# Optimization experiments

Measured on AMD Instinct MI355X. Metric: run time of the kernel, lower is better.

Reference implementation:

```python
import jax, jax.numpy as jnp
import numpy as np

BS, TS, NE, ED = 32, 64, 64, 96
E = 256        # attn_embed_dim
H = 4          # attn_n_heads
HD = E // H    # head dim
RNN_H = 256
N_ACT = 32
NA = 16        # n_agents


def setup_inputs():
    key = jax.random.key(0)
    ks = jax.random.split(key, 40)
    entities = jax.random.normal(ks[0], (BS, TS, NE, ED), jnp.float32)
    obs_mask = jax.random.randint(ks[1], (BS, TS, NE, NE), 0, 2).astype(jnp.float32)  # 1 = masked
    entity_mask = (jax.random.uniform(ks[2], (BS, TS, NE)) < 0.1).astype(jnp.float32)  # 1 = inactive
    hidden_state = jnp.zeros((BS * NA, RNN_H), jnp.float32)
    it = iter(range(3, 40))
    def lin(fi, fo):
        return jax.random.normal(ks[next(it)], (fi, fo), jnp.float32) / np.sqrt(fi).astype(np.float32)
    p = dict(
        fc1_w=lin(ED, E), fc1_b=jnp.zeros((E,), jnp.float32),
        attn_in_w=lin(E, 3 * E), attn_out_w=lin(E, E), attn_out_b=jnp.zeros((E,), jnp.float32),
        fc2_w=lin(2 * E, RNN_H), fc2_b=jnp.zeros((RNN_H,), jnp.float32),
        gru_w_ih=lin(RNN_H, 3 * RNN_H), gru_w_hh=lin(RNN_H, 3 * RNN_H),
        gru_b_ih=jnp.zeros((3 * RNN_H,), jnp.float32), gru_b_hh=jnp.zeros((3 * RNN_H,), jnp.float32),
        fc3_w=lin(RNN_H, N_ACT), fc3_b=jnp.zeros((N_ACT,), jnp.float32),
        fcmsg1_w=lin(ED, E), fcmsg1_b=jnp.zeros((E,), jnp.float32),
        lmsg_in_w=lin(E, 3 * E), lmsg_out_w=lin(E, E), lmsg_out_b=jnp.zeros((E,), jnp.float32),
        gmsg_in_w=lin(E, 3 * E), gmsg_out_w=lin(E, E), gmsg_out_b=jnp.zeros((E,), jnp.float32),
        gate_in_w=lin(E, 3 * E), gate_out_w=lin(E, E), gate_out_b=jnp.zeros((E,), jnp.float32),
        gatefc1_w=lin(ED, E), gatefc1_b=jnp.zeros((E,), jnp.float32),
        gatefc2_w=lin(E, 2), gatefc2_b=jnp.zeros((2,), jnp.float32),
    )
    return dict(entities=entities, obs_mask=obs_mask, entity_mask=entity_mask,
                hidden_state=hidden_state, **p)


def _attn(x, in_w, out_w, out_b, pre_mask, post_mask):
    """REFIL EntityAttentionLayer: n_queries = NA agent rows, masks use 1 = masked."""
    B, ne, e = x.shape
    q, k, v = jnp.split(x @ in_w, 3, axis=-1)                       # each [B, ne, E]
    q = q[:, :NA].reshape(B, NA, H, HD).transpose(0, 2, 1, 3)        # [B, H, NA, HD]
    k = k.reshape(B, ne, H, HD).transpose(0, 2, 1, 3)                # [B, H, ne, HD]
    v = v.reshape(B, ne, H, HD).transpose(0, 2, 1, 3)
    logits = jnp.einsum('bhqd,bhkd->bhqk', q, k) / jnp.asarray(np.sqrt(HD), x.dtype)
    m = pre_mask[:, None, :NA, :]                                    # [B, 1, NA, ne]
    logits = jnp.where(m > 0, jnp.asarray(-1e9, x.dtype), logits)
    # softmax; zeroing masked cols also reproduces torch's NaN->0 for fully-masked rows
    w = jax.nn.softmax(logits, axis=-1) * (1.0 - m)
    out = jnp.einsum('bhqk,bhkd->bhqd', w, v).transpose(0, 2, 1, 3).reshape(B, NA, e)
    out = out @ out_w + out_b
    return out * (1.0 - post_mask[..., None])                        # masked_fill(post_mask, 0)


def _forward(entities, obs_mask, entity_mask, hidden_state,
             fc1_w, fc1_b, attn_in_w, attn_out_w, attn_out_b, fc2_w, fc2_b,
             gru_w_ih, gru_w_hh, gru_b_ih, gru_b_hh, fc3_w, fc3_b,
             fcmsg1_w, fcmsg1_b, lmsg_in_w, lmsg_out_w, lmsg_out_b,
             gmsg_in_w, gmsg_out_w, gmsg_out_b, gate_in_w, gate_out_w, gate_out_b,
             gatefc1_w, gatefc1_b, gatefc2_w, gatefc2_b):
    bs, ts, ne, ed = entities.shape
    B = bs * ts
    ent = entities.reshape(B, ne, ed)
    om = obs_mask.reshape(B, ne, ne)
    em = entity_mask.reshape(B, ne)
    agent_mask = em[:, :NA]                                          # [B, NA]
    full_obs_mask = 1.0 - (1.0 - agent_mask[:, None, :]) * (1.0 - agent_mask[:, :, None])

    x1 = jax.nn.relu(ent @ fc1_w + fc1_b)
    x2 = _attn(x1, attn_in_w, attn_out_w, attn_out_b, om, agent_mask)          # [B, NA, E]

    x1_msg = jax.nn.relu(ent @ fcmsg1_w + fcmsg1_b)
    x1_gate = jax.nn.relu(ent @ gatefc1_w + gatefc1_b)
    x2_msg = _attn(x1_msg, lmsg_in_w, lmsg_out_w, lmsg_out_b, om, agent_mask)  # [B, NA, E]
    x2_gate = _attn(x1_gate, gate_in_w, gate_out_w, gate_out_b, om, agent_mask)
    x2_gate = x2_gate @ gatefc2_w + gatefc2_b                                   # [B, NA, 2]

    # argmax of softmax == argmax of logits; gate in {0,1}, non-differentiable
    gate = jnp.argmax(x2_gate, axis=-1).astype(entities.dtype)
    gated_msg = x2_msg * gate[..., None]
    global_msg = _attn(gated_msg, gmsg_in_w, gmsg_out_w, gmsg_out_b,
                       full_obs_mask, agent_mask)                               # [B, NA, E]

    x3 = jax.nn.relu(jnp.concatenate([x2, global_msg], axis=-1) @ fc2_w + fc2_b)
    x3 = x3.reshape(bs, ts, NA, RNN_H)

    # GRU recurrence over ts via scan; hidden flattened to [bs*NA, RNN_H]
    h0 = hidden_state.reshape(-1, RNN_H)
    xs = x3.transpose(1, 0, 2, 3).reshape(ts, bs * NA, RNN_H)

    def step(h, x):
        gi = x @ gru_w_ih + gru_b_ih
        gh = h @ gru_w_hh + gru_b_hh
        ir, iz, inn = jnp.split(gi, 3, axis=-1)
        hr, hz, hn = jnp.split(gh, 3, axis=-1)
        r = jax.nn.sigmoid(ir + hr)
        z = jax.nn.sigmoid(iz + hz)
        n = jnp.tanh(inn + r * hn)
        h_new = (1.0 - z) * n + z * h
        return h_new, h_new

    _, hs = jax.lax.scan(step, h0, xs)                               # [ts, bs*NA, RNN_H]
    hs = hs.reshape(ts, bs, NA, RNN_H).transpose(1, 0, 2, 3)         # [bs, ts, NA, RNN_H]

    q = hs @ fc3_w + fc3_b                                           # [bs, ts, NA, N_ACT]
    am = agent_mask.reshape(bs, ts, NA, 1)
    q = q * (1.0 - am)                                               # masked_fill(agent_mask, 0)
    return q, hs, x2_gate


def reference(entities, obs_mask, entity_mask, hidden_state,
              fc1_w, fc1_b, attn_in_w, attn_out_w, attn_out_b, fc2_w, fc2_b,
              gru_w_ih, gru_w_hh, gru_b_ih, gru_b_hh, fc3_w, fc3_b,
              fcmsg1_w, fcmsg1_b, lmsg_in_w, lmsg_out_w, lmsg_out_b,
              gmsg_in_w, gmsg_out_w, gmsg_out_b, gate_in_w, gate_out_w, gate_out_b,
              gatefc1_w, gatefc1_b, gatefc2_w, gatefc2_b):
    return _forward(entities, obs_mask, entity_mask, hidden_state,
                    fc1_w, fc1_b, attn_in_w, attn_out_w, attn_out_b, fc2_w, fc2_b,
                    gru_w_ih, gru_w_hh, gru_b_ih, gru_b_hh, fc3_w, fc3_b,
                    fcmsg1_w, fcmsg1_b, lmsg_in_w, lmsg_out_w, lmsg_out_b,
                    gmsg_in_w, gmsg_out_w, gmsg_out_b, gate_in_w, gate_out_w, gate_out_b,
                    gatefc1_w, gatefc1_b, gatefc2_w, gatefc2_b)
```

## Files before the change

kernel.cpp:

```cpp
#include <hip/hip_runtime.h>


#define DEV __device__ __forceinline__

typedef _Float16 f16x8 __attribute__((ext_vector_type(8)));
typedef _Float16 f16x4 __attribute__((ext_vector_type(4)));
typedef float    f32x4 __attribute__((ext_vector_type(4)));
typedef float    f32x16 __attribute__((ext_vector_type(16)));

DEV f32x4 mfma16(f16x8 a, f16x8 b, f32x4 c){
  return __builtin_amdgcn_mfma_f32_16x16x32_f16(a, b, c, 0, 0, 0);
}
DEV f32x16 mfma32(f16x8 a, f16x8 b, f32x16 c){
  return __builtin_amdgcn_mfma_f32_32x32x16_f16(a, b, c, 0, 0, 0);
}

template<int MODE> struct AB {
  f16x8 hi, lo;
  DEV void mf(const AB& b, f32x4& c) const {
    if constexpr (MODE){
      c = mfma16(lo, b.hi, c);
      c = mfma16(hi, b.lo, c);
    }
    c = mfma16(hi, b.hi, c);
  }
};

template<int MODE> DEV AB<MODE> ldW(const _Float16* p, int losz){
  AB<MODE> r; r.hi = *(const f16x8*)p;
  if constexpr (MODE) r.lo = *(const f16x8*)(p + losz);
  return r;
}
template<int MODE> DEV AB<MODE> ldL(const _Float16* ph, const _Float16* pl){
  AB<MODE> r; r.hi = *(const f16x8*)ph;
  if constexpr (MODE) r.lo = *(const f16x8*)pl;
  return r;
}
template<int MODE> DEV AB<MODE> ldF(const float* p){
  AB<MODE> r;
  f32x4 v0 = *(const f32x4*)p, v1 = *(const f32x4*)(p + 4);
#pragma unroll
  for (int i = 0; i < 4; ++i){
    float a = v0[i], b = v1[i];
    _Float16 ah = (_Float16)a, bh = (_Float16)b;
    r.hi[i] = ah; r.hi[i+4] = bh;
    if constexpr (MODE){
      r.lo[i]   = (_Float16)(a - (float)ah);
      r.lo[i+4] = (_Float16)(b - (float)bh);
    }
  }
  return r;
}
template<int MODE> DEV void stL(_Float16* ph, _Float16* pl, int idx, float v){
  _Float16 h = (_Float16)v;
  ph[idx] = h;
  if constexpr (MODE) pl[idx] = (_Float16)(v - (float)h);
}

struct WJobs {
  const float* src[15];
  unsigned off[15];
  int K[15], N[15], mode[15];
};

__global__ __launch_bounds__(256) void k0_conv(WJobs jb, char* ws){
  const int job = blockIdx.y;
  const int K = jb.K[job], N = jb.N[job];
  const int total = K * N;
  _Float16* dh = (_Float16*)(ws + jb.off[job]);
  const float* src = jb.src[job];
  const int m = jb.mode[job];
  for (int idx = blockIdx.x*256 + threadIdx.x; idx < total; idx += gridDim.x*256){
    int n = idx / K, k = idx - n*K;
    float v = src[(size_t)k*N + n];
    _Float16 h = (_Float16)v;
    dh[idx] = h;
    if (m) dh[total + idx] = (_Float16)(v - (float)h);
  }
}

__global__ __launch_bounds__(256) void k0w_gate(
    const float* __restrict__ Wout, const float* __restrict__ Wg2,
    const float* __restrict__ bo,   const float* __restrict__ Win,
    _Float16* __restrict__ wveff, float* __restrict__ beff)
{
  __shared__ float weff_s[256*2];
  const int tid = threadIdx.x;
  {
    float a0 = 0.f, a1 = 0.f;
    const float* wr = Wout + (size_t)tid*256;
    for (int f = 0; f < 256; ++f){ float x = wr[f]; a0 += x*Wg2[2*f]; a1 += x*Wg2[2*f+1]; }
    weff_s[tid*2] = a0; weff_s[tid*2+1] = a1;
  }
  if (tid < 2){
    float s = 0.f;
    for (int f = 0; f < 256; ++f) s += bo[f]*Wg2[2*f + tid];
    beff[tid] = s;
  }
  __syncthreads();
  {
    const int j = tid;
    for (int n = 0; n < 16; ++n){
      float v = 0.f;
      if (n < 8){
        int h = n >> 1, c = n & 1;
        const float* wr = Win + (size_t)j*768 + 512 + h*64;
        const float* we = weff_s + (h*64)*2 + c;
        for (int d = 0; d < 64; ++d) v += wr[d]*we[2*d];
      }
      _Float16 hi = (_Float16)v;
      wveff[n*256 + j] = hi;
      wveff[16*256 + n*256 + j] = (_Float16)(v - (float)hi);
    }
  }
}

__global__ __launch_bounds__(512) void k1_all(
    const float* __restrict__ ent, const float* __restrict__ om, const float* __restrict__ em,
    const _Float16* __restrict__ W1a, const float* __restrict__ b1a,
    const _Float16* __restrict__ WINa,
    const _Float16* __restrict__ WOUTa, const float* __restrict__ boa,
    float* __restrict__ x2outa,
    const _Float16* __restrict__ W1b, const float* __restrict__ b1b,
    const _Float16* __restrict__ WINb,
    const _Float16* __restrict__ WOUTb, const float* __restrict__ bob,
    float* __restrict__ x2outb,
    const _Float16* __restrict__ W1g, const float* __restrict__ b1g,
    const _Float16* __restrict__ WINg,
    const _Float16* __restrict__ WVEFF,
    const float* __restrict__ beff, const float* __restrict__ gb2,
    float* __restrict__ og, float* __restrict__ gate)
{
  const int tid = threadIdx.x;
  const int w = tid >> 6, lg = (tid >> 4) & 3, li = tid & 15;
  extern __shared__ char smem[];

  if (blockIdx.x < 2048){
    const int br = blockIdx.x >> 10;
    const int p  = blockIdx.x & 1023;
    const int bb2[2] = { 2*p, 2*p + 1 };
    const _Float16* W1   = br ? W1b   : W1a;
    const float*    b1   = br ? b1b   : b1a;
    const _Float16* WIN  = br ? WINb  : WINa;
    const _Float16* WOUT = br ? WOUTb : WOUTa;
    const float*    bo   = br ? bob   : boa;
    float*          x2out= br ? x2outb: x2outa;

    const int wi = w & 3, ih = w >> 2;
    const int l = tid & 63;
    const int r32 = l & 31, kh = (l >> 5)*8;

    _Float16* x1  = (_Float16*)smem;
    _Float16* Ks  = (_Float16*)(smem + 67584);
    _Float16* Vs  = (_Float16*)(smem + 86016);
    _Float16* Qs  = (_Float16*)(smem + 104448);
    float*    lgs = (float*)(smem + 109056);
    _Float16* Ps  = (_Float16*)(smem + 118272);
    float*    outp= (float*)(smem + 122880);

    {
      const int b = bb2[ih];
      _Float16* x1p = x1 + ih*16896;
      const int mt = wi & 1, ntb = (wi >> 1)*4;
      f32x16 acc0 = 0.f, acc1 = 0.f, acc2 = 0.f, acc3 = 0.f;
#pragma unroll
      for (int kk = 0; kk < 6; ++kk){
        AB<0> a = ldF<0>(ent + ((size_t)b*64 + mt*32 + r32)*96 + kk*16 + kh);
        f16x8 B0 = *(const f16x8*)(W1 + (size_t)((ntb + 0)*32 + r32)*96 + kk*16 + kh);
        f16x8 B1 = *(const f16x8*)(W1 + (size_t)((ntb + 1)*32 + r32)*96 + kk*16 + kh);
        f16x8 B2 = *(const f16x8*)(W1 + (size_t)((ntb + 2)*32 + r32)*96 + kk*16 + kh);
        f16x8 B3 = *(const f16x8*)(W1 + (size_t)((ntb + 3)*32 + r32)*96 + kk*16 + kh);
        acc0 = mfma32(a.hi, B0, acc0);
        acc1 = mfma32(a.hi, B1, acc1);
        acc2 = mfma32(a.hi, B2, acc2);
        acc3 = mfma32(a.hi, B3, acc3);
      }
#pragma unroll
      for (int s = 0; s < 4; ++s){
        const f32x16& ac = (s == 0) ? acc0 : (s == 1) ? acc1 : (s == 2) ? acc2 : acc3;
        int col = (ntb + s)*32 + r32;
        float bias = b1[col];
#pragma unroll
        for (int reg = 0; reg < 16; ++reg){
          int row = (reg & 3) + 8*(reg >> 2) + 4*(l >> 5);
          x1p[(mt*32 + row)*264 + col] = (_Float16)fmaxf(ac[reg] + bias, 0.f);
        }
      }
    }
    __syncthreads();

    for (int h = 0; h < 4; ++h){
      if (w < 4){
        const int kt = w >> 1, dt = w & 1;
        f32x16 acc0 = 0.f, acc1 = 0.f;
        for (int kk = 0; kk < 16; ++kk){
          int ao = (kt*32 + r32)*264 + kk*16 + kh;
          f16x8 A0 = *(const f16x8*)(x1 + ao);
          f16x8 A1 = *(const f16x8*)(x1 + 16896 + ao);
          f16x8 B = *(const f16x8*)(WIN + (size_t)(256 + 64*h + dt*32 + r32)*256 + kk*16 + kh);
          acc0 = mfma32(A0, B, acc0);
          acc1 = mfma32(A1, B, acc1);
        }
#pragma unroll
        for (int reg = 0; reg < 16; ++reg){
          int row = (reg & 3) + 8*(reg >> 2) + 4*(l >> 5);
          Ks[(kt*32 + row)*72 + dt*32 + r32]        = (_Float16)acc0[reg];
          Ks[4608 + (kt*32 + row)*72 + dt*32 + r32] = (_Float16)acc1[reg];
        }
      } else {
        const int wv = w - 4;
        const int kt = wv >> 1, dt = wv & 1;
        f32x16 acc0 = 0.f, acc1 = 0.f;
        for (int kk = 0; kk < 16; ++kk){
          int ao = (kt*32 + r32)*264 + kk*16 + kh;
          f16x8 A0 = *(const f16x8*)(x1 + ao);
          f16x8 A1 = *(const f16x8*)(x1 + 16896 + ao);
          f16x8 B = *(const f16x8*)(WIN + (size_t)(512 + 64*h + dt*32 + r32)*256 + kk*16 + kh);
          acc0 = mfma32(A0, B, acc0);
          acc1 = mfma32(A1, B, acc1);
        }
#pragma unroll
        for (int rr = 0; rr < 4; ++rr){
          f16x4 p0, p1;
#pragma unroll
          for (int q4 = 0; q4 < 4; ++q4){
            p0[q4] = (_Float16)acc0[rr*4 + q4];
            p1[q4] = (_Float16)acc1[rr*4 + q4];
          }
          int key = kt*32 + rr*8 + 4*(l >> 5);
          *(f16x4*)(Vs + (dt*32 + r32)*72 + key)        = p0;
          *(f16x4*)(Vs + 4608 + (dt*32 + r32)*72 + key) = p1;
        }
      }
      {
        f32x4 acc = 0.f;
        for (int kk = 0; kk < 8; ++kk){
          f16x8 A = *(const f16x8*)(x1 + ih*16896 + li*264 + kk*32 + lg*8);
          f16x8 B = *(const f16x8*)(WIN + (size_t)(64*h + 16*wi + li)*256 + kk*32 + lg*8);
          acc = mfma16(A, B, acc);
        }
#pragma unroll
        for (int j = 0; j < 4; ++j)
          Qs[ih*1152 + (4*lg + j)*72 + 16*wi + li] = (_Float16)acc[j];
      }
      __syncthreads();
      {
        const int b = bb2[ih];
        f32x4 acc = 0.f;
#pragma unroll
        for (int kk = 0; kk < 2; ++kk){
          f16x8 A = *(const f16x8*)(Qs + ih*1152 + li*72 + kk*32 + lg*8);
          f16x8 B = *(const f16x8*)(Ks + ih*4608 + (16*wi + li)*72 + kk*32 + lg*8);
          acc = mfma16(A, B, acc);
        }
#pragma unroll
        for (int j = 0; j < 4; ++j){
          int q = 4*lg + j, key = 16*wi + li;
          float v = acc[j] * 0.125f;
          float m = om[((size_t)b*64 + q)*64 + key];
          if (m > 0.f) v = -1e9f;
          lgs[ih*1152 + q*72 + key] = v;
        }
      }
      __syncthreads();
      {
        const int it = tid >> 8, q = (tid >> 4) & 15, i16 = tid & 15;
        const int b = bb2[it];
        float pv[4], mx = -3e38f;
#pragma unroll
        for (int u = 0; u < 4; ++u){ pv[u] = lgs[it*1152 + q*72 + i16 + 16*u]; mx = fmaxf(mx, pv[u]); }
#pragma unroll
        for (int d = 1; d < 16; d <<= 1) mx = fmaxf(mx, __shfl_xor(mx, d, 16));
        float s = 0.f;
#pragma unroll
        for (int u = 0; u < 4; ++u){ pv[u] = expf(pv[u] - mx); s += pv[u]; }
#pragma unroll
        for (int d = 1; d < 16; d <<= 1) s += __shfl_xor(s, d, 16);
#pragma unroll
        for (int u = 0; u < 4; ++u){
          int key = i16 + 16*u;
          float m = om[((size_t)b*64 + q)*64 + key];
          Ps[it*1152 + q*72 + key] = (_Float16)((pv[u]/s)*(1.f - m));
        }
      }
      __syncthreads();
      {
        f32x4 acc = 0.f;
#pragma unroll
        for (int kk = 0; kk < 2; ++kk){
          f16x8 A = *(const f16x8*)(Ps + ih*1152 + li*72 + kk*32 + lg*8);
          f16x8 B = *(const f16x8*)(Vs + ih*4608 + (16*wi + li)*72 + kk*32 + lg*8);
          acc = mfma16(A, B, acc);
        }
#pragma unroll
        for (int j = 0; j < 4; ++j)
          outp[ih*4224 + (4*lg + j)*264 + 64*h + 16*wi + li] = acc[j];
      }
      __syncthreads();
    }

    {
      f32x4 acc[2][2];
#pragma unroll
      for (int it = 0; it < 2; ++it)
#pragma unroll
        for (int c = 0; c < 2; ++c) acc[it][c] = 0.f;
      for (int kk = 0; kk < 8; ++kk){
        AB<0> a0 = ldF<0>(outp + li*264 + kk*32 + lg*8);
        AB<0> a1 = ldF<0>(outp + 4224 + li*264 + kk*32 + lg*8);
#pragma unroll
        for (int cc = 0; cc < 2; ++cc){
          int c = 2*ih + cc;
          f16x8 B = *(const f16x8*)(WOUT + (size_t)(64*wi + 16*c + li)*256 + kk*32 + lg*8);
          acc[0][cc] = mfma16(a0.hi, B, acc[0][cc]);
          acc[1][cc] = mfma16(a1.hi, B, acc[1][cc]);
        }
      }
#pragma unroll
      for (int it = 0; it < 2; ++it){
        const int b = bb2[it];
#pragma unroll
        for (int cc = 0; cc < 2; ++cc){
          int col = 64*wi + 16*(2*ih + cc) + li;
          float bias = bo[col];
#pragma unroll
          for (int j = 0; j < 4; ++j){
            int q = 4*lg + j;
            float v = (acc[it][cc][j] + bias) * (1.f - em[(size_t)b*64 + q]);
            x2out[((size_t)b*16 + q)*256 + col] = v;
          }
        }
      }
    }
    return;
  }

  {
    constexpr int W1SZ = 96*256, WINSZ = 256*768, WVSZ = 16*256;
    const int b = blockIdx.x - 2048;
    const int l = tid & 63;
    const int r32 = l & 31, kh = (l >> 5)*8;

    char* sp = smem;
    _Float16* x1h = (_Float16*)sp; sp += 64*264*2;
    _Float16* x1l = (_Float16*)sp; sp += 64*264*2;
    _Float16* Kh  = (_Float16*)sp; sp += 64*72*2;
    _Float16* Kl  = (_Float16*)sp; sp += 64*72*2;
    _Float16* Qh  = (_Float16*)sp; sp += 16*264*2;
    _Float16* Ql  = (_Float16*)sp; sp += 16*264*2;
    float*    lgs = (float*)sp;    sp += 16*72*4;
    float*    Ps  = (float*)sp;    sp += 16*66*4;
    float*    v2s = (float*)sp;    sp += 64*18*4;
    float*  ogacc = (float*)sp;    sp += 32*4;
    float*  Kpart = (float*)sp;    sp += 8192*4;

    {
      const int mt = w & 1, ntb = (w >> 1)*2;
      f32x16 acc0 = 0.f, acc1 = 0.f;
#pragma unroll
      for (int kk = 0; kk < 6; ++kk){
        AB<1> a = ldF<1>(ent + ((size_t)b*64 + mt*32 + r32)*96 + kk*16 + kh);
#pragma unroll
        for (int s = 0; s < 2; ++s){
          const _Float16* bp = W1g + (size_t)((ntb + s)*32 + r32)*96 + kk*16 + kh;
          f16x8 Bh = *(const f16x8*)bp;
          f16x8 Bl = *(const f16x8*)(bp + W1SZ);
          f32x16& ac = s ? acc1 : acc0;
          ac = mfma32(a.lo, Bh, ac);
          ac = mfma32(a.hi, Bl, ac);
          ac = mfma32(a.hi, Bh, ac);
        }
      }
#pragma unroll
      for (int s = 0; s < 2; ++s){
        const f32x16& ac = s ? acc1 : acc0;
        int col = (ntb + s)*32 + r32;
        float bias = b1g[col];
#pragma unroll
        for (int reg = 0; reg < 16; ++reg){
          int row = (reg & 3) + 8*(reg >> 2) + 4*(l >> 5);
          stL<1>(x1h, x1l, (mt*32 + row)*264 + col, fmaxf(ac[reg] + bias, 0.f));
        }
      }
    }
    if (tid < 32) ogacc[tid] = 0.f;
    __syncthreads();

    {
#pragma unroll
      for (int s = 0; s < 2; ++s){
        int nt = w + s*8;
        f32x4 acc = 0.f;
        for (int kk = 0; kk < 8; ++kk){
          int ao = li*264 + kk*32 + lg*8;
          AB<1> a = ldL<1>(x1h + ao, x1l + ao);
          AB<1> bb = ldW<1>(WINg + (size_t)(nt*16 + li)*256 + kk*32 + lg*8, WINSZ);
          a.mf(bb, acc);
        }
#pragma unroll
        for (int j = 0; j < 4; ++j)
          stL<1>(Qh, Ql, (4*lg + j)*264 + nt*16 + li, acc[j]);
      }
      if (w < 4){
        f32x4 acc = 0.f;
        for (int kk = 0; kk < 8; ++kk){
          int ao = (w*16 + li)*264 + kk*32 + lg*8;
          AB<1> a = ldL<1>(x1h + ao, x1l + ao);
          AB<1> bb = ldW<1>(WVEFF + (size_t)li*256 + kk*32 + lg*8, WVSZ);
          a.mf(bb, acc);
        }
#pragma unroll
        for (int j = 0; j < 4; ++j)
          v2s[(w*16 + 4*lg + j)*18 + li] = acc[j];
      }
    }
    __syncthreads();

    for (int h = 0; h < 4; ++h){
      {
        const int t = w & 3, kt = t >> 1, dt = t & 1, khalf = w >> 2;
        f32x16 acc = 0.f;
#pragma unroll
        for (int k8 = 0; k8 < 8; ++k8){
          int ko = (khalf*8 + k8)*16 + kh;
          int ao = (kt*32 + r32)*264 + ko;
          f16x8 ah = *(const f16x8*)(x1h + ao);
          f16x8 al = *(const f16x8*)(x1l + ao);
          const _Float16* bp = WINg + (size_t)(256 + h*64 + dt*32 + r32)*256 + ko;
          f16x8 Bh = *(const f16x8*)bp;
          f16x8 Bl = *(const f16x8*)(bp + WINSZ);
          acc = mfma32(al, Bh, acc);
          acc = mfma32(ah, Bl, acc);
          acc = mfma32(ah, Bh, acc);
        }
#pragma unroll
        for (int reg = 0; reg < 16; ++reg){
          int row = (reg & 3) + 8*(reg >> 2) + 4*(l >> 5);
          Kpart[((khalf*4 + t)*32 + row)*32 + r32] = acc[reg];
        }
      }
      __syncthreads();
      {
        for (int e = tid; e < 4096; e += 512){
          float s2 = Kpart[e] + Kpart[4096 + e];
          int t2 = e >> 10, idx = e & 1023, row = idx >> 5, col = idx & 31;
          stL<1>(Kh, Kl, ((t2 >> 1)*32 + row)*72 + (t2 & 1)*32 + col, s2);
        }
      }
      __syncthreads();
      if (w < 4){
        f32x4 acc = 0.f;
#pragma unroll
        for (int kk = 0; kk < 2; ++kk){
          int ao = li*264 + h*64 + kk*32 + lg*8;
          AB<1> a = ldL<1>(Qh + ao, Ql + ao);
          int bo_ = (16*w + li)*72 + kk*32 + lg*8;
          AB<1> bb = ldL<1>(Kh + bo_, Kl + bo_);
          a.mf(bb, acc);
        }
#pragma unroll
        for (int j = 0; j < 4; ++j){
          int q = 4*lg + j, key = 16*w + li;
          float v = acc[j] * 0.125f;
          float m = om[((size_t)b*64 + q)*64 + key];
          if (m > 0.f) v = -1e9f;
          lgs[q*72 + key] = v;
        }
      }
      __syncthreads();
      if (tid < 256){
        int q = tid >> 4, i16 = tid & 15;
        float pv[4], mx = -3e38f;
#pragma unroll
        for (int u = 0; u < 4; ++u){ pv[u] = lgs[q*72 + i16 + 16*u]; mx = fmaxf(mx, pv[u]); }
#pragma unroll
        for (int d = 1; d < 16; d <<= 1) mx = fmaxf(mx, __shfl_xor(mx, d, 16));
        float s = 0.f;
#pragma unroll
        for (int u = 0; u < 4; ++u){ pv[u] = expf(pv[u] - mx); s += pv[u]; }
#pragma unroll
        for (int d = 1; d < 16; d <<= 1) s += __shfl_xor(s, d, 16);
#pragma unroll
        for (int u = 0; u < 4; ++u){
          int key = i16 + 16*u;
          float m = om[((size_t)b*64 + q)*64 + key];
          Ps[q*66 + key] = (pv[u]/s)*(1.f - m);
        }
      }
      __syncthreads();
      if (tid < 256){
        int q = tid >> 4, l16 = tid & 15;
        float a0 = 0.f, a1 = 0.f;
#pragma unroll
        for (int u = 0; u < 4; ++u){
          int k = l16 + 16*u;
          float p2 = Ps[q*66 + k];
          a0 += p2 * v2s[k*18 + h*2];
          a1 += p2 * v2s[k*18 + h*2 + 1];
        }
#pragma unroll
        for (int d = 1; d < 16; d <<= 1){ a0 += __shfl_xor(a0, d, 16); a1 += __shfl_xor(a1, d, 16); }
        if (l16 == 0){ ogacc[q*2] += a0; ogacc[q*2 + 1] += a1; }
      }
      __syncthreads();
    }
    if (tid < 16){
      int q = tid;
      float am = em[(size_t)b*64 + q];
      float g0 = (1.f - am)*(ogacc[2*q]     + beff[0]) + gb2[0];
      float g1 = (1.f - am)*(ogacc[2*q + 1] + beff[1]) + gb2[1];
      og[((size_t)b*16 + q)*2]     = g0;
      og[((size_t)b*16 + q)*2 + 1] = g1;
      gate[(size_t)b*16 + q] = (g1 > g0) ? 1.f : 0.f;
    }
  }
}

__global__ __launch_bounds__(256) void k2_global(
    const float* __restrict__ em,
    const float* __restrict__ x2, const float* __restrict__ x2m,
    const float* __restrict__ gate,
    const _Float16* __restrict__ GMIN, const _Float16* __restrict__ GMOUT, const float* __restrict__ gob,
    const _Float16* __restrict__ FC2T, const float* __restrict__ fc2b,
    const _Float16* __restrict__ GIHT, const float* __restrict__ gib,
    float* __restrict__ gi)
{
  const int p = blockIdx.x;
  const int tid = threadIdx.x;
  const int w = tid >> 6, lg = (tid >> 4) & 3, li = tid & 15;

  extern __shared__ char smem[];
  float*    gate_s = (float*)smem;
  _Float16* gm_s   = (_Float16*)(smem + 128);
  _Float16* Q2     = (_Float16*)(smem + 17024);
  _Float16* K2s    = (_Float16*)(smem + 21632);
  _Float16* Vt2    = (_Float16*)(smem + 26240);
  float*    lg2    = (float*)(smem + 36480);
  _Float16* P2     = (_Float16*)(smem + 39552);
  _Float16* outp   = (_Float16*)(smem + 42112);
  _Float16* cat_s  = (_Float16*)(smem + 59008);
  _Float16* x3_s   = (_Float16*)(smem + 92288);

  if (tid < 32){
    int it = tid >> 4, q = tid & 15;
    gate_s[it*16 + q] = gate[(size_t)(2*p + it)*16 + q];
  }
  __syncthreads();
#pragma unroll
  for (int it = 0; it < 2; ++it){
    const int b = 2*p + it;
    for (int idx = tid; idx < 4096; idx += 256){
      int q = idx >> 8, d = idx & 255;
      gm_s[it*4224 + q*264 + d]  = (_Float16)(x2m[((size_t)b*16 + q)*256 + d] * gate_s[it*16 + q]);
      cat_s[it*8320 + q*520 + d] = (_Float16)(x2[((size_t)b*16 + q)*256 + d]);
    }
  }
  for (int idx = tid; idx < 2*64*40; idx += 256) Vt2[idx] = (_Float16)0.f;
  for (int idx = tid; idx < 2*16*40; idx += 256) P2[idx] = (_Float16)0.f;
  __syncthreads();
  for (int h = 0; h < 4; ++h){
    {
      f32x4 aq0 = 0.f, aq1 = 0.f, ak0 = 0.f, ak1 = 0.f, av0 = 0.f, av1 = 0.f;
      for (int kk = 0; kk < 8; ++kk){
        f16x8 A0 = *(const f16x8*)(gm_s + li*264 + kk*32 + lg*8);
        f16x8 A1 = *(const f16x8*)(gm_s + 4224 + li*264 + kk*32 + lg*8);
        f16x8 Bq = *(const f16x8*)(GMIN + (size_t)(      64*h + 16*w + li)*256 + kk*32 + lg*8);
        f16x8 Bk = *(const f16x8*)(GMIN + (size_t)(256 + 64*h + 16*w + li)*256 + kk*32 + lg*8);
        f16x8 Bv = *(const f16x8*)(GMIN + (size_t)(512 + 64*h + 16*w + li)*256 + kk*32 + lg*8);
        aq0 = mfma16(A0, Bq, aq0); aq1 = mfma16(A1, Bq, aq1);
        ak0 = mfma16(A0, Bk, ak0); ak1 = mfma16(A1, Bk, ak1);
        av0 = mfma16(A0, Bv, av0); av1 = mfma16(A1, Bv, av1);
      }
#pragma unroll
      for (int j = 0; j < 4; ++j){
        int rw = 4*lg + j, dim = 16*w + li;
        Q2[rw*72 + dim]         = (_Float16)aq0[j];
        Q2[1152 + rw*72 + dim]  = (_Float16)aq1[j];
        K2s[rw*72 + dim]        = (_Float16)ak0[j];
        K2s[1152 + rw*72 + dim] = (_Float16)ak1[j];
        Vt2[dim*40 + rw]        = (_Float16)av0[j];
        Vt2[2560 + dim*40 + rw] = (_Float16)av1[j];
      }
    }
    __syncthreads();
    if (w < 2){
      const int it = w, b = 2*p + it;
      f32x4 acc = 0.f;
#pragma unroll
      for (int kk = 0; kk < 2; ++kk){
        f16x8 A = *(const f16x8*)(Q2  + it*1152 + li*72 + kk*32 + lg*8);
        f16x8 B = *(const f16x8*)(K2s + it*1152 + li*72 + kk*32 + lg*8);
        acc = mfma16(A, B, acc);
      }
      float amk = em[(size_t)b*64 + li];
#pragma unroll
      for (int j = 0; j < 4; ++j){
        int q = 4*lg + j;
        float amq = em[(size_t)b*64 + q];
        float m = 1.f - (1.f - amq)*(1.f - amk);
        float v = acc[j]*0.125f;
        if (m > 0.f) v = -1e9f;
        lg2[it*384 + q*24 + li] = v;
      }
    }
    __syncthreads();
    {
      int q = tid >> 4, key = tid & 15;
#pragma unroll
      for (int it = 0; it < 2; ++it){
        const int b = 2*p + it;
        float v = lg2[it*384 + q*24 + key];
        float mx = v;
#pragma unroll
        for (int d = 1; d < 16; d <<= 1) mx = fmaxf(mx, __shfl_xor(mx, d, 16));
        float pe = expf(v - mx);
        float s = pe;
#pragma unroll
        for (int d = 1; d < 16; d <<= 1) s += __shfl_xor(s, d, 16);
        float amq = em[(size_t)b*64 + q], amk = em[(size_t)b*64 + key];
        float m = 1.f - (1.f - amq)*(1.f - amk);
        P2[it*640 + q*40 + key] = (_Float16)((pe/s)*(1.f - m));
      }
    }
    __syncthreads();
    {
#pragma unroll
      for (int it = 0; it < 2; ++it){
        f32x4 acc = 0.f;
        f16x8 A = *(const f16x8*)(P2 + it*640 + li*40 + lg*8);
        f16x8 B = *(const f16x8*)(Vt2 + it*2560 + (16*w + li)*40 + lg*8);
        acc = mfma16(A, B, acc);
#pragma unroll
        for (int j = 0; j < 4; ++j)
          outp[it*4224 + (4*lg + j)*264 + 64*h + 16*w + li] = (_Float16)acc[j];
      }
    }
    __syncthreads();
  }
  {
#pragma unroll
    for (int c = 0; c < 4; ++c){
      int col = 64*w + 16*c + li;
      f32x4 a0 = 0.f, a1 = 0.f;
      for (int kk = 0; kk < 8; ++kk){
        f16x8 B  = *(const f16x8*)(GMOUT + (size_t)col*256 + kk*32 + lg*8);
        f16x8 A0 = *(const f16x8*)(outp + li*264 + kk*32 + lg*8);
        f16x8 A1 = *(const f16x8*)(outp + 4224 + li*264 + kk*32 + lg*8);
        a0 = mfma16(A0, B, a0);
        a1 = mfma16(A1, B, a1);
      }
      float bias = gob[col];
#pragma unroll
      for (int j = 0; j < 4; ++j){
        int q = 4*lg + j;
        float m0 = 1.f - em[(size_t)(2*p)*64 + q];
        float m1 = 1.f - em[(size_t)(2*p + 1)*64 + q];
        cat_s[q*520 + 256 + col]        = (_Float16)((a0[j] + bias)*m0);
        cat_s[8320 + q*520 + 256 + col] = (_Float16)((a1[j] + bias)*m1);
      }
    }
  }
  __syncthreads();
  {
#pragma unroll
    for (int c = 0; c < 4; ++c){
      int col = 64*w + 16*c + li;
      f32x4 a0 = 0.f, a1 = 0.f;
      for (int kk = 0; kk < 16; ++kk){
        f16x8 B  = *(const f16x8*)(FC2T + (size_t)col*512 + kk*32 + lg*8);
        f16x8 A0 = *(const f16x8*)(cat_s + li*520 + kk*32 + lg*8);
        f16x8 A1 = *(const f16x8*)(cat_s + 8320 + li*520 + kk*32 + lg*8);
        a0 = mfma16(A0, B, a0);
        a1 = mfma16(A1, B, a1);
      }
      float bias = fc2b[col];
#pragma unroll
      for (int j = 0; j < 4; ++j){
        x3_s[(4*lg + j)*264 + col]        = (_Float16)fmaxf(a0[j] + bias, 0.f);
        x3_s[4224 + (4*lg + j)*264 + col] = (_Float16)fmaxf(a1[j] + bias, 0.f);
      }
    }
  }
  __syncthreads();
  {
    const int r0 = ((2*p) >> 6)*16, t0 = (2*p) & 63;
#pragma unroll
    for (int cc = 0; cc < 12; ++cc){
      int col = (w*12 + cc)*16 + li;
      f32x4 a0 = 0.f, a1 = 0.f;
      for (int kk = 0; kk < 8; ++kk){
        f16x8 B  = *(const f16x8*)(GIHT + (size_t)col*256 + kk*32 + lg*8);
        f16x8 A0 = *(const f16x8*)(x3_s + li*264 + kk*32 + lg*8);
        f16x8 A1 = *(const f16x8*)(x3_s + 4224 + li*264 + kk*32 + lg*8);
        a0 = mfma16(A0, B, a0);
        a1 = mfma16(A1, B, a1);
      }
      float bias = gib[col];
#pragma unroll
      for (int j = 0; j < 4; ++j){
        int q = 4*lg + j;
        gi[((size_t)((r0 + q)*64 + t0))*768 + col]     = a0[j] + bias;
        gi[((size_t)((r0 + q)*64 + t0 + 1))*768 + col] = a1[j] + bias;
      }
    }
  }
}

__global__ __launch_bounds__(256) void k3_gru(
    const _Float16* __restrict__ WHH, const float* __restrict__ bhh,
    const float* __restrict__ gi, const float* __restrict__ h0,
    float* __restrict__ hs)
{
  const int rb = blockIdx.x;
  const int row0 = rb * 16;
  const int tid = threadIdx.x;
  const int w = tid >> 6, lg = (tid >> 4) & 3, li = tid & 15;

  extern __shared__ char smem3[];
  _Float16* hf16 = (_Float16*)smem3;
  float* hf32 = (float*)(smem3 + 8448);
  float* gh   = (float*)(smem3 + 8448 + 16640);
  float* bhs  = (float*)(smem3 + 8448 + 16640 + 49664);

  for (int idx = tid; idx < 768; idx += 256) bhs[idx] = bhh[idx];
  for (int idx = tid; idx < 4096; idx += 256){
    int r = idx >> 8, d = idx & 255;
    float v = h0[(size_t)(row0 + r)*256 + d];
    hf32[r*260 + d] = v;
    hf16[r*264 + d] = (_Float16)v;
  }
  __syncthreads();

  const int er = tid >> 4;
  const int d0 = (tid & 15) * 16;

  for (int t = 0; t < 64; ++t){
    const float* gp = gi + ((size_t)(row0 + er)*64 + t)*768 + d0;
    f32x4 gr[4], gz[4], gn[4];
#pragma unroll
    for (int v = 0; v < 4; ++v){
      gr[v] = *(const f32x4*)(gp + v*4);
      gz[v] = *(const f32x4*)(gp + 256 + v*4);
      gn[v] = *(const f32x4*)(gp + 512 + v*4);
    }
    f16x8 a[8];
#pragma unroll
    for (int kk = 0; kk < 8; ++kk)
      a[kk] = *(const f16x8*)(hf16 + li*264 + kk*32 + lg*8);
    f32x4 acc[12];
#pragma unroll
    for (int c = 0; c < 12; ++c) acc[c] = 0.f;
#pragma unroll
    for (int c = 0; c < 12; ++c){
      const _Float16* bp = WHH + (size_t)(w*192 + c*16 + li)*256 + lg*8;
#pragma unroll
      for (int kk = 0; kk < 8; ++kk)
        acc[c] = mfma16(a[kk], *(const f16x8*)(bp + kk*32), acc[c]);
    }
#pragma unroll
    for (int c = 0; c < 12; ++c){
      int col = w*192 + c*16 + li;
#pragma unroll
      for (int j = 0; j < 4; ++j)
        gh[(4*lg + j)*776 + col] = acc[c][j];
    }
    __syncthreads();
    {
      float* hp32 = hf32 + er*260 + d0;
      float* hsp  = hs + ((size_t)(rb*64 + t)*16 + er)*256 + d0;
      f16x8 hv8[2];
#pragma unroll
      for (int v = 0; v < 4; ++v){
        f32x4 xr = *(const f32x4*)(gh + er*776 +       d0 + v*4);
        f32x4 xz = *(const f32x4*)(gh + er*776 + 256 + d0 + v*4);
        f32x4 xn = *(const f32x4*)(gh + er*776 + 512 + d0 + v*4);
        f32x4 hold = *(const f32x4*)(hp32 + v*4);
        f32x4 hout;
#pragma unroll
        for (int e = 0; e < 4; ++e){
          int d = d0 + v*4 + e;
          float rr_ = 1.f/(1.f + __expf(-(gr[v][e] + xr[e] + bhs[d])));
          float zz  = 1.f/(1.f + __expf(-(gz[v][e] + xz[e] + bhs[256 + d])));
          float pre = gn[v][e] + rr_*(xn[e] + bhs[512 + d]);
          float nn  = 1.f - 2.f/(1.f + __expf(2.f*pre));
          float hv = (1.f - zz)*nn + zz*hold[e];
          hout[e] = hv;
          int sl = v*4 + e;
          hv8[sl >> 3][sl & 7] = (_Float16)hv;
        }
        *(f32x4*)(hp32 + v*4) = hout;
        *(f32x4*)(hsp + v*4)  = hout;
      }
      *(f16x8*)(hf16 + er*264 + d0)     = hv8[0];
      *(f16x8*)(hf16 + er*264 + d0 + 8) = hv8[1];
    }
    __syncthreads();
  }
}

__global__ __launch_bounds__(256) void k4_q(
    const _Float16* __restrict__ FC3T, const float* __restrict__ fc3b,
    const float* __restrict__ em, const float* __restrict__ hs, float* __restrict__ qo)
{
  const int tid = threadIdx.x;
  const int w = tid >> 6, lg = (tid >> 4) & 3, li = tid & 15;
  const int rb = blockIdx.x*64 + 16*w;
  f32x4 acc[2];
#pragma unroll
  for (int c = 0; c < 2; ++c) acc[c] = 0.f;
  for (int kk = 0; kk < 8; ++kk){
    const float* ap = hs + (size_t)(rb + li)*256 + kk*32 + lg*8;
    f32x4 v0 = *(const f32x4*)ap, v1 = *(const f32x4*)(ap + 4);
    f16x8 A;
#pragma unroll
    for (int e = 0; e < 4; ++e){ A[e] = (_Float16)v0[e]; A[e+4] = (_Float16)v1[e]; }
#pragma unroll
    for (int c = 0; c < 2; ++c){
      f16x8 B = *(const f16x8*)(FC3T + (size_t)(16*c + li)*256 + kk*32 + lg*8);
      acc[c] = mfma16(A, B, acc[c]);
    }
  }
#pragma unroll
  for (int c = 0; c < 2; ++c){
    int col = 16*c + li;
    float bias = fc3b[col];
#pragma unroll
    for (int j = 0; j < 4; ++j){
      int row = rb + 4*lg + j;
      float am = em[(size_t)(row >> 4)*64 + (row & 15)];
      qo[(size_t)row*32 + col] = (acc[c][j] + bias)*(1.f - am);
    }
  }
}

extern "C" void kernel_launch(void* const* d_in, const int* in_sizes, int n_in,
                              void* d_out, int out_size, void* d_ws, size_t ws_size,
                              hipStream_t stream)
{
  constexpr size_t OFF_FC1T   = 0;
  constexpr size_t OFF_MSG1T  = 49152;
  constexpr size_t OFF_AINT   = 98304;
  constexpr size_t OFF_LINT   = 491520;
  constexpr size_t OFF_AOUTT  = 884736;
  constexpr size_t OFF_LOUTT  = 1015808;
  constexpr size_t OFF_GMINT  = 1146880;
  constexpr size_t OFF_GMOUTT = 1540096;
  constexpr size_t OFF_FC2T   = 1671168;
  constexpr size_t OFF_GIHT   = 1933312;
  constexpr size_t OFF_GHHT   = 2326528;
  constexpr size_t OFF_FC3T   = 2719744;
  constexpr size_t OFF_G1T    = 2736128;
  constexpr size_t OFF_GINT   = 2834432;
  constexpr size_t OFF_WVEFF  = 3620864;
  constexpr size_t OFF_BEFF   = 3637248;
  constexpr size_t OFF_GATE   = 3637504;
  constexpr size_t OFF_X2     = 3768576;
  constexpr size_t OFF_X2M    = 37323008;
  constexpr size_t OFF_GI     = 70877440;
  constexpr size_t NEED       = 171540736;
  if (ws_size < NEED) return;

  char* ws = (char*)d_ws;
  const float* ent = (const float*)d_in[0];
  const float* om  = (const float*)d_in[1];
  const float* em  = (const float*)d_in[2];

  WJobs jb{};
  int nj = 0;
  auto addj = [&](int src_idx, size_t off, int K, int N, int m){
    jb.src[nj] = (const float*)d_in[src_idx]; jb.off[nj] = (unsigned)off;
    jb.K[nj] = K; jb.N[nj] = N; jb.mode[nj] = m; ++nj;
  };
  addj(4,  OFF_FC1T,   96, 256, 0);
  addj(17, OFF_MSG1T,  96, 256, 0);
  addj(6,  OFF_AINT,  256, 768, 0);
  addj(19, OFF_LINT,  256, 768, 0);
  addj(7,  OFF_AOUTT, 256, 256, 0);
  addj(20, OFF_LOUTT, 256, 256, 0);
  addj(22, OFF_GMINT, 256, 768, 0);
  addj(23, OFF_GMOUTT,256, 256, 0);
  addj(9,  OFF_FC2T,  512, 256, 0);
  addj(11, OFF_GIHT,  256, 768, 0);
  addj(12, OFF_GHHT,  256, 768, 0);
  addj(15, OFF_FC3T,  256,  32, 0);
  addj(28, OFF_G1T,    96, 256, 1);
  addj(25, OFF_GINT,  256, 768, 1);
  k0_conv<<<dim3(96, nj), 256, 0, stream>>>(jb, ws);

  k0w_gate<<<1, 256, 0, stream>>>(
      (const float*)d_in[26], (const float*)d_in[30],
      (const float*)d_in[27], (const float*)d_in[25],
      (_Float16*)(ws + OFF_WVEFF), (float*)(ws + OFF_BEFF));

  constexpr int SMB = 156672, SMK2 = 109184, SM3 = 77824;
  (void)hipFuncSetAttribute(reinterpret_cast<const void*>(&k1_all),
                            hipFuncAttributeMaxDynamicSharedMemorySize, SMB);
  (void)hipFuncSetAttribute(reinterpret_cast<const void*>(&k2_global),
                            hipFuncAttributeMaxDynamicSharedMemorySize, SMK2);
  (void)hipFuncSetAttribute(reinterpret_cast<const void*>(&k3_gru),
                            hipFuncAttributeMaxDynamicSharedMemorySize, SM3);

  float* qout = (float*)d_out;
  float* hsout = qout + 1048576;
  float* gout = qout + 9437184;

  k1_all<<<4096, 512, SMB, stream>>>(ent, om, em,
      (const _Float16*)(ws + OFF_FC1T),  (const float*)d_in[5],
      (const _Float16*)(ws + OFF_AINT),
      (const _Float16*)(ws + OFF_AOUTT), (const float*)d_in[8],
      (float*)(ws + OFF_X2),
      (const _Float16*)(ws + OFF_MSG1T), (const float*)d_in[18],
      (const _Float16*)(ws + OFF_LINT),
      (const _Float16*)(ws + OFF_LOUTT), (const float*)d_in[21],
      (float*)(ws + OFF_X2M),
      (const _Float16*)(ws + OFF_G1T),   (const float*)d_in[29],
      (const _Float16*)(ws + OFF_GINT),
      (const _Float16*)(ws + OFF_WVEFF),
      (const float*)(ws + OFF_BEFF), (const float*)d_in[31],
      gout, (float*)(ws + OFF_GATE));

  k2_global<<<1024, 256, SMK2, stream>>>(em,
      (const float*)(ws + OFF_X2), (const float*)(ws + OFF_X2M),
      (const float*)(ws + OFF_GATE),
      (const _Float16*)(ws + OFF_GMINT), (const _Float16*)(ws + OFF_GMOUTT), (const float*)d_in[24],
      (const _Float16*)(ws + OFF_FC2T), (const float*)d_in[10],
      (const _Float16*)(ws + OFF_GIHT), (const float*)d_in[13],
      (float*)(ws + OFF_GI));

  k3_gru<<<32, 256, SM3, stream>>>(
      (const _Float16*)(ws + OFF_GHHT), (const float*)d_in[14],
      (const float*)(ws + OFF_GI), (const float*)d_in[3], hsout);

  k4_q<<<512, 256, 0, stream>>>(
      (const _Float16*)(ws + OFF_FC3T), (const float*)d_in[16],
      em, hsout, qout);
}
```

Baseline: 1.333 ms.

## Hoist Q projection out of head loop and use 32x32 MFMA for out-proj

The Q projection for all heads is computed once, right after fc1, into a full shared-memory Q buffer using 32x32x16 MFMAs. This replaces the per-head 16x16 Q computation inside the head loop. The attention output buffer is now stored as fp16 instead of fp32, and the output projection runs as one 32x32 MFMA tile per wave over both batch items. The intent is to cut per-head MFMA work and shared-memory traffic in the loop, at the cost of more shared memory, an extra barrier, and slightly lower precision on the attention output.

```diff
diff --git a/kernel.cpp b/kernel.cpp
--- a/kernel.cpp
+++ b/kernel.cpp
@@ -150,13 +150,13 @@
     const int l = tid & 63;
     const int r32 = l & 31, kh = (l >> 5)*8;
 
-    _Float16* x1  = (_Float16*)smem;
-    _Float16* Ks  = (_Float16*)(smem + 67584);
-    _Float16* Vs  = (_Float16*)(smem + 86016);
-    _Float16* Qs  = (_Float16*)(smem + 104448);
-    float*    lgs = (float*)(smem + 109056);
-    _Float16* Ps  = (_Float16*)(smem + 118272);
-    float*    outp= (float*)(smem + 122880);
+    _Float16* x1   = (_Float16*)smem;
+    _Float16* Ks   = (_Float16*)(smem + 67584);
+    _Float16* Vs   = (_Float16*)(smem + 86016);
+    _Float16* Qful = (_Float16*)(smem + 104448);
+    float*    lgs  = (float*)(smem + 121344);
+    _Float16* Ps   = (_Float16*)(smem + 130560);
+    _Float16* outp = (_Float16*)(smem + 135168);
 
     {
       const int b = bb2[ih];
@@ -185,6 +185,22 @@
           int row = (reg & 3) + 8*(reg >> 2) + 4*(l >> 5);
           x1p[(mt*32 + row)*264 + col] = (_Float16)fmaxf(ac[reg] + bias, 0.f);
         }
+      }
+    }
+    __syncthreads();
+
+    {
+      f32x16 acc = 0.f;
+      const int itq = r32 >> 4, qr = r32 & 15;
+      for (int kk = 0; kk < 16; ++kk){
+        f16x8 A = *(const f16x8*)(x1 + itq*16896 + qr*264 + kk*16 + kh);
+        f16x8 B = *(const f16x8*)(WIN + (size_t)(w*32 + r32)*256 + kk*16 + kh);
+        acc = mfma32(A, B, acc);
+      }
+#pragma unroll
+      for (int reg = 0; reg < 16; ++reg){
+        int row = (reg & 3) + 8*(reg >> 2) + 4*(l >> 5);
+        Qful[(row >> 4)*4224 + (row & 15)*264 + w*32 + r32] = (_Float16)acc[reg];
       }
     }
     __syncthreads();
@@ -232,24 +248,13 @@
           *(f16x4*)(Vs + 4608 + (dt*32 + r32)*72 + key) = p1;
         }
       }
-      {
-        f32x4 acc = 0.f;
-        for (int kk = 0; kk < 8; ++kk){
-          f16x8 A = *(const f16x8*)(x1 + ih*16896 + li*264 + kk*32 + lg*8);
-          f16x8 B = *(const f16x8*)(WIN + (size_t)(64*h + 16*wi + li)*256 + kk*32 + lg*8);
-          acc = mfma16(A, B, acc);
-        }
-#pragma unroll
-        for (int j = 0; j < 4; ++j)
-          Qs[ih*1152 + (4*lg + j)*72 + 16*wi + li] = (_Float16)acc[j];
-      }
       __syncthreads();
       {
         const int b = bb2[ih];
         f32x4 acc = 0.f;
 #pragma unroll
         for (int kk = 0; kk < 2; ++kk){
-          f16x8 A = *(const f16x8*)(Qs + ih*1152 + li*72 + kk*32 + lg*8);
+          f16x8 A = *(const f16x8*)(Qful + ih*4224 + li*264 + 64*h + kk*32 + lg*8);
           f16x8 B = *(const f16x8*)(Ks + ih*4608 + (16*wi + li)*72 + kk*32 + lg*8);
           acc = mfma16(A, B, acc);
         }
@@ -294,42 +299,28 @@
         }
 #pragma unroll
         for (int j = 0; j < 4; ++j)
-          outp[ih*4224 + (4*lg + j)*264 + 64*h + 16*wi + li] = acc[j];
+          outp[ih*4224 + (4*lg + j)*264 + 64*h + 16*wi + li] = (_Float16)acc[j];
       }
       __syncthreads();
     }
 
     {
-      f32x4 acc[2][2];
-#pragma unroll
-      for (int it = 0; it < 2; ++it)
-#pragma unroll
-        for (int c = 0; c < 2; ++c) acc[it][c] = 0.f;
-      for (int kk = 0; kk < 8; ++kk){
-        AB<0> a0 = ldF<0>(outp + li*264 + kk*32 + lg*8);
-        AB<0> a1 = ldF<0>(outp + 4224 + li*264 + kk*32 + lg*8);
-#pragma unroll
-        for (int cc = 0; cc < 2; ++cc){
-          int c = 2*ih + cc;
-          f16x8 B = *(const f16x8*)(WOUT + (size_t)(64*wi + 16*c + li)*256 + kk*32 + lg*8);
-          acc[0][cc] = mfma16(a0.hi, B, acc[0][cc]);
-          acc[1][cc] = mfma16(a1.hi, B, acc[1][cc]);
-        }
-      }
-#pragma unroll
-      for (int it = 0; it < 2; ++it){
-        const int b = bb2[it];
-#pragma unroll
-        for (int cc = 0; cc < 2; ++cc){
-          int col = 64*wi + 16*(2*ih + cc) + li;
-          float bias = bo[col];
-#pragma unroll
-          for (int j = 0; j < 4; ++j){
-            int q = 4*lg + j;
-            float v = (acc[it][cc][j] + bias) * (1.f - em[(size_t)b*64 + q]);
-            x2out[((size_t)b*16 + q)*256 + col] = v;
-          }
-        }
+      f32x16 acc = 0.f;
+      const int ito = r32 >> 4, qr = r32 & 15;
+      for (int kk = 0; kk < 16; ++kk){
+        f16x8 A = *(const f16x8*)(outp + ito*4224 + qr*264 + kk*16 + kh);
+        f16x8 B = *(const f16x8*)(WOUT + (size_t)(w*32 + r32)*256 + kk*16 + kh);
+        acc = mfma32(A, B, acc);
+      }
+      int col = w*32 + r32;
+      float bias = bo[col];
+#pragma unroll
+      for (int reg = 0; reg < 16; ++reg){
+        int row = (reg & 3) + 8*(reg >> 2) + 4*(l >> 5);
+        int it2 = row >> 4, q2 = row & 15;
+        const int b = bb2[it2];
+        float v = (acc[reg] + bias) * (1.f - em[(size_t)b*64 + q2]);
+        x2out[((size_t)b*16 + q2)*256 + col] = v;
       }
     }
     return;
```

Result: no change. 1.312 ms (-1.5%).
